# Performance work log

Hardware: AMD Instinct MI355X
Metric: run time of the kernel (lower is better)

## Reference

```python
import jax, jax.numpy as jnp
import numpy as np

N = 50000          # number of nodes / output rows (len(degs))
IN_C, OUT_C = 16, 16
EDGE_F = 13        # edge feature dim fed to filter net
HID = 32           # filter-net hidden width
E_NOMINAL = 800000 # target number of edges (sum of degs)


def setup_inputs() -> dict:
    rng = np.random.default_rng(0)
    # variable per-node degrees in [0, 32], adjusted so they sum exactly to E_NOMINAL
    degs = rng.integers(0, 33, size=N).astype(np.int64)
    degs[0] = max(0, degs[0] + (E_NOMINAL - int(degs.sum())))
    E = int(degs.sum())
    # segment id of each edge = destination node (equivalent to the degs-driven loop)
    idxd = np.repeat(np.arange(N, dtype=np.int32), degs)
    idxn = rng.integers(0, N, size=E).astype(np.int32)  # source node gather index

    key = jax.random.key(0)
    k1, k2, k3, k4 = jax.random.split(key, 4)
    x = jax.random.normal(k1, (N, IN_C), jnp.float32)
    edgefeats = jax.random.normal(k2, (E, EDGE_F), jnp.float32)
    # filter net: Linear(EDGE_F->HID) -> ReLU -> Linear(HID->IN_C*OUT_C)
    W1 = jax.random.normal(k3, (EDGE_F, HID), jnp.float32) / np.float32(np.sqrt(EDGE_F))
    b1 = jnp.zeros((HID,), jnp.float32)
    W2 = jax.random.normal(k4, (HID, IN_C * OUT_C), jnp.float32) / np.float32(np.sqrt(HID))
    b2 = jnp.zeros((IN_C * OUT_C,), jnp.float32)
    return {
        "x": x, "edgefeats": edgefeats,
        "W1": W1, "b1": b1, "W2": W2, "b2": b2,
        "idxn": jnp.asarray(idxn), "idxd": jnp.asarray(idxd),
        "degs": jnp.asarray(degs.astype(np.float32)),
    }


def reference(x, edgefeats, W1, b1, W2, b2, idxn, idxd, degs):
    # filter net generates a per-edge [IN_C, OUT_C] weight matrix
    h = jax.nn.relu(edgefeats @ W1 + b1)                 # [E, HID]
    w = (h @ W2 + b2).reshape(-1, IN_C, OUT_C)           # [E, IN_C, OUT_C]
    # gather source-node features and apply per-edge matvec (bmm with [E,1,IN_C])
    sel = x[idxn]                                        # [E, IN_C]
    prod = jnp.einsum('ei,eio->eo', sel, w)              # [E, OUT_C]
    # segment-mean over each node's incoming edges; degree-0 nodes -> 0
    s = jax.ops.segment_sum(prod, idxd, num_segments=N)  # [N, OUT_C]
    d = degs[:, None]
    return jnp.where(d > 0, s / jnp.maximum(d, 1.0), jnp.float32(0.0))
```

## Files before the change

### kernel.cpp

```cpp
#include <hip/hip_runtime.h>

typedef _Float16 half2v __attribute__((ext_vector_type(2)));
typedef _Float16 half4v __attribute__((ext_vector_type(4)));
typedef _Float16 half8v __attribute__((ext_vector_type(8)));
typedef float   float4v __attribute__((ext_vector_type(4)));

#define INC     16
#define OUTC    16
#define EFN     13
#define HIDC    32
#define EPB     128
#define MAXSPAN 80

#define GLOBAL_AS __attribute__((address_space(1)))
#define LDS_AS    __attribute__((address_space(3)))

union H8 { half8v v; half2v h2[4]; };

__global__ __launch_bounds__(256) void prep(
    const float* __restrict__ W2,
    const float* __restrict__ x,
    _Float16*    __restrict__ wsB,
    _Float16*    __restrict__ wsXh,
    int nh)
{
    const int b = blockIdx.x;
    if (b < 32) {
        const int i = b * 256 + threadIdx.x;
        const int j = i & 7;
        const int l = (i >> 3) & 63;
        const int t = i >> 9;
        const int q = l >> 4, n = l & 15;
        const int kk = (j < 4) ? (q * 4 + j) : (16 + q * 4 + (j & 3));
        wsB[i] = (_Float16)W2[kk * 256 + t * 16 + n];
    } else {
        const int i = (b - 32) * 256 + threadIdx.x;
        if (i * 8 < nh) {
            const float4 v0 = ((const float4*)x)[i * 2];
            const float4 v1 = ((const float4*)x)[i * 2 + 1];
            half8v h;
            h[0] = (_Float16)v0.x; h[1] = (_Float16)v0.y;
            h[2] = (_Float16)v0.z; h[3] = (_Float16)v0.w;
            h[4] = (_Float16)v1.x; h[5] = (_Float16)v1.y;
            h[6] = (_Float16)v1.z; h[7] = (_Float16)v1.w;
            *(half8v*)(wsXh + (size_t)i * 8) = h;
        }
    }
}

__global__ __launch_bounds__(64, 3) void edge_kernel(
    const _Float16* __restrict__ xh,
    const float* __restrict__ edgefeats,
    const float* __restrict__ W1,
    const float* __restrict__ b1,
    const float* __restrict__ b2,
    const int*   __restrict__ idxn,
    const int*   __restrict__ idxd,
    const float* __restrict__ degs,
    const _Float16* __restrict__ wsB,
    float*       __restrict__ out,
    float*       __restrict__ wsPfirst,
    float*       __restrict__ wsPlast,
    int*         __restrict__ wsMeta,
    int E)
{
    __shared__ __align__(16) float sEF[EPB * EFN];
    __shared__ __align__(16) int   sidxn[EPB];
    __shared__ __align__(16) int   sidxd[EPB];
    __shared__ float lacc[MAXSPAN * OUTC];

    const int lane = threadIdx.x;
    const int n    = lane & 15;
    const int q    = lane >> 4;

    const long b0   = (long)blockIdx.x * EPB;
    const long bEnd = (b0 + EPB < (long)E) ? (b0 + EPB) : (long)E;
    const bool full = (b0 + EPB <= (long)E);

    if (full) {
        const char* efsrc = (const char*)edgefeats + (size_t)b0 * (EFN * 4);
        #pragma unroll
        for (int c = 0; c < 6; ++c)
            __builtin_amdgcn_global_load_lds(
                (const GLOBAL_AS unsigned int*)(efsrc + c * 1024 + lane * 16),
                (LDS_AS unsigned int*)((char*)sEF + c * 1024), 16, 0, 0);
        if (lane < 32) {
            __builtin_amdgcn_global_load_lds(
                (const GLOBAL_AS unsigned int*)(efsrc + 6144 + lane * 16),
                (LDS_AS unsigned int*)((char*)sEF + 6144), 16, 0, 0);
            __builtin_amdgcn_global_load_lds(
                (const GLOBAL_AS unsigned int*)((const char*)(idxn + b0) + lane * 16),
                (LDS_AS unsigned int*)sidxn, 16, 0, 0);
            __builtin_amdgcn_global_load_lds(
                (const GLOBAL_AS unsigned int*)((const char*)(idxd + b0) + lane * 16),
                (LDS_AS unsigned int*)sidxd, 16, 0, 0);
        }
    } else {
        const long mx = (long)E * EFN - 1;
        for (int i = lane; i < EPB * EFN; i += 64) {
            long gi = b0 * EFN + i;
            if (gi > mx) gi = mx;
            sEF[i] = edgefeats[gi];
        }
        const long Ec = (long)E - 1;
        for (int i = lane; i < EPB; i += 64) {
            long e = b0 + i;
            if (e > Ec) e = Ec;
            sidxn[i] = idxn[e];
            sidxd[i] = idxd[e];
        }
    }

    const int d_lo = idxd[b0];
    const int d_hi = idxd[bEnd - 1];
    const int span = d_hi - d_lo;

    H8 bfr[16];
    #pragma unroll
    for (int t = 0; t < 16; ++t)
        bfr[t].v = *(const half8v*)(wsB + ((size_t)(t * 64 + lane) * 8));

    #pragma unroll
    for (int it = 0; it < MAXSPAN * OUTC / 64; ++it) lacc[lane + it * 64] = 0.0f;

    half4v a1, a2;
    float4v c1, c2;
    #pragma unroll
    for (int jj = 0; jj < 4; ++jj) {
        const int f = q * 4 + jj;
        const bool ok = (f < EFN);
        a1[jj] = ok ? (_Float16)W1[f * HIDC + n]      : (_Float16)0.f;
        a2[jj] = ok ? (_Float16)W1[f * HIDC + 16 + n] : (_Float16)0.f;
        c1[jj] = b1[q * 4 + jj];
        c2[jj] = b1[16 + q * 4 + jj];
    }
    half8v bfragB2;
    #pragma unroll
    for (int j = 0; j < 8; ++j) {
        _Float16 val = (_Float16)0.f;
        if (q < 2) val = (_Float16)b2[(q * 8 + j) * 16 + n];
        bfragB2[j] = val;
    }

    const int f0i = (q < 3) ? (q * 4) : 9;

    __syncthreads();

    const int nd0 = sidxn[n];
    const int nd1 = sidxn[16 + n];
    half8v pxa0 = *(const half8v*)(xh + (size_t)nd0 * INC);
    half8v pxb0 = *(const half8v*)(xh + (size_t)nd0 * INC + 8);
    half8v pxa1 = *(const half8v*)(xh + (size_t)nd1 * INC);
    half8v pxb1 = *(const half8v*)(xh + (size_t)nd1 * INC + 8);
    __builtin_amdgcn_sched_barrier(0);

    #pragma unroll
    for (int t16 = 0; t16 < 8; ++t16) {
        const long base = b0 + (long)t16 * 16;
        const bool vM   = (base + n < (long)E);

        const half8v xA = (t16 & 1) ? pxa1 : pxa0;
        const half8v xB = (t16 & 1) ? pxb1 : pxb0;
        if (t16 < 6) {
            const int ndn = sidxn[(t16 + 2) * 16 + n];
            if (t16 & 1) {
                pxa1 = *(const half8v*)(xh + (size_t)ndn * INC);
                pxb1 = *(const half8v*)(xh + (size_t)ndn * INC + 8);
            } else {
                pxa0 = *(const half8v*)(xh + (size_t)ndn * INC);
                pxb0 = *(const half8v*)(xh + (size_t)ndn * INC + 8);
            }
        }
        __builtin_amdgcn_sched_barrier(0);

        const int4 dd = *(const int4*)&sidxd[t16 * 16 + q * 4];

        const float* efp = sEF + (size_t)(t16 * 16 + n) * EFN + f0i;
        const float e0 = efp[0], e1 = efp[1], e2 = efp[2], e3 = efp[3];

        H8 sa, sb_;
        sa.v = xA; sb_.v = xB;
        const half2v zz = {(_Float16)0.f, (_Float16)0.f};
        half2v selh[8];
        #pragma unroll
        for (int i = 0; i < 4; ++i) {
            selh[i]     = vM ? sa.h2[i]  : zz;
            selh[4 + i] = vM ? sb_.h2[i] : zz;
        }

        half4v efB;
        if (q < 3) {
            efB[0] = (_Float16)e0; efB[1] = (_Float16)e1;
            efB[2] = (_Float16)e2; efB[3] = (_Float16)e3;
        } else {
            efB[0] = (_Float16)e3; efB[1] = (_Float16)0.f;
            efB[2] = (_Float16)0.f; efB[3] = (_Float16)0.f;
        }

        const float4v hf1 = __builtin_amdgcn_mfma_f32_16x16x16f16(a1, efB, c1, 0, 0, 0);
        const float4v hf2 = __builtin_amdgcn_mfma_f32_16x16x16f16(a2, efB, c2, 0, 0, 0);

        H8 hu;
        #pragma unroll
        for (int r = 0; r < 2; ++r) {
            half2v t1 = {(_Float16)fmaxf(hf1[2*r], 0.f), (_Float16)fmaxf(hf1[2*r+1], 0.f)};
            half2v t2 = {(_Float16)fmaxf(hf2[2*r], 0.f), (_Float16)fmaxf(hf2[2*r+1], 0.f)};
            hu.h2[r]     = t1;
            hu.h2[2 + r] = t2;
        }

        float4v acc = {0.f, 0.f, 0.f, 0.f};
        #pragma unroll
        for (int t = 0; t < 16; ++t) {
            _Float16 sv = (t & 1) ? selh[t >> 1][1] : selh[t >> 1][0];
            half2v sb = {sv, sv};
            H8 a;
            a.h2[0] = sb * hu.h2[0];
            a.h2[1] = sb * hu.h2[1];
            a.h2[2] = sb * hu.h2[2];
            a.h2[3] = sb * hu.h2[3];
            acc = __builtin_amdgcn_mfma_f32_16x16x32_f16(a.v, bfr[t].v, acc, 0, 0, 0);
        }
        {
            H8 a;
            #pragma unroll
            for (int j2 = 0; j2 < 4; ++j2) {
                a.h2[j2] = (q < 2) ? selh[q * 4 + j2] : zz;
            }
            acc = __builtin_amdgcn_mfma_f32_16x16x32_f16(a.v, bfragB2, acc, 0, 0, 0);
        }

        if (dd.x == dd.w) {
            atomicAdd(&lacc[(dd.x - d_lo) * OUTC + n],
                      acc[0] + acc[1] + acc[2] + acc[3]);
        } else {
            atomicAdd(&lacc[(dd.x - d_lo) * OUTC + n], acc[0]);
            atomicAdd(&lacc[(dd.y - d_lo) * OUTC + n], acc[1]);
            atomicAdd(&lacc[(dd.z - d_lo) * OUTC + n], acc[2]);
            atomicAdd(&lacc[(dd.w - d_lo) * OUTC + n], acc[3]);
        }
    }

    __syncthreads();

    const bool first_starts = (b0 == 0)        || (idxd[b0 - 1] != d_lo);
    const bool last_ends    = (bEnd == (long)E) || (idxd[bEnd]   != d_hi);

    for (int i = lane; i < (span + 1) * OUTC; i += 64) {
        const int u = i >> 4;
        const int o = i & 15;
        const int v = d_lo + u;
        const float bin = lacc[u * OUTC + o];
        const bool starts = (u > 0)    || first_starts;
        const bool ends   = (u < span) || last_ends;
        if (starts && ends) {
            const float dg = degs[v];
            out[(size_t)v * OUTC + o] = (dg > 0.0f) ? bin / dg : 0.0f;
        } else if (!starts) {
            wsPfirst[(size_t)blockIdx.x * OUTC + o] = bin;
        } else {
            wsPlast[(size_t)blockIdx.x * OUTC + o] = bin;
        }
    }
    if (lane == 0) {
        wsMeta[blockIdx.x * 4 + 0] = d_hi;
        wsMeta[blockIdx.x * 4 + 1] = last_ends ? 1 : 0;
        wsMeta[blockIdx.x * 4 + 2] =
            (((span > 0) || first_starts) && !last_ends) ? 1 : 0;
    }
}

__global__ __launch_bounds__(256) void fixup_kernel(
    const float* __restrict__ degs,
    float*       __restrict__ out,
    const float* __restrict__ wsPfirst,
    const float* __restrict__ wsPlast,
    const int*   __restrict__ wsMeta,
    int N, int nblocks)
{
    const int t = blockIdx.x * 256 + threadIdx.x;

    if (t < nblocks && wsMeta[t * 4 + 2]) {
        const int v = wsMeta[t * 4 + 0];
        float tot[OUTC];
        #pragma unroll
        for (int o = 0; o < OUTC; ++o) tot[o] = wsPlast[(size_t)t * OUTC + o];
        for (int j = t + 1; j < nblocks; ++j) {
            #pragma unroll
            for (int o = 0; o < OUTC; ++o) tot[o] += wsPfirst[(size_t)j * OUTC + o];
            if (wsMeta[j * 4 + 0] != v || wsMeta[j * 4 + 1]) break;
        }
        const float dg = degs[v];
        #pragma unroll
        for (int o = 0; o < OUTC; ++o) out[(size_t)v * OUTC + o] = tot[o] / dg;
    }

    if (t < N && degs[t] == 0.0f) {
        float4* op = (float4*)(out + (size_t)t * OUTC);
        const float4 z = make_float4(0, 0, 0, 0);
        op[0] = z; op[1] = z; op[2] = z; op[3] = z;
    }
}

extern "C" void kernel_launch(void* const* d_in, const int* in_sizes, int n_in,
                              void* d_out, int out_size, void* d_ws, size_t ws_size,
                              hipStream_t stream)
{
    const float* x         = (const float*)d_in[0];
    const float* edgefeats = (const float*)d_in[1];
    const float* W1        = (const float*)d_in[2];
    const float* b1        = (const float*)d_in[3];
    const float* W2        = (const float*)d_in[4];
    const float* b2        = (const float*)d_in[5];
    const int*   idxn      = (const int*)d_in[6];
    const int*   idxd      = (const int*)d_in[7];
    const float* degs      = (const float*)d_in[8];

    const int E = in_sizes[6];
    const int N = in_sizes[8];
    const int nblocks = (E + EPB - 1) / EPB;
    const int nh = N * INC;

    _Float16* wsB  = (_Float16*)d_ws;
    _Float16* wsXh = (_Float16*)((char*)d_ws + 16384);
    size_t xh_bytes = ((size_t)nh * 2 + 255) & ~(size_t)255;
    float* wsPfirst = (float*)((char*)d_ws + 16384 + xh_bytes);
    float* wsPlast  = wsPfirst + (size_t)nblocks * OUTC;
    int*   wsMeta   = (int*)(wsPlast + (size_t)nblocks * OUTC);

    const int xhblocks = (nh / 8 + 255) / 256;
    prep<<<32 + xhblocks, 256, 0, stream>>>(W2, x, wsB, wsXh, nh);

    edge_kernel<<<nblocks, 64, 0, stream>>>(wsXh, edgefeats, W1, b1, b2,
                                            idxn, idxd, degs, wsB, (float*)d_out,
                                            wsPfirst, wsPlast, wsMeta, E);

    const int fthreads = (N > nblocks) ? N : nblocks;
    fixup_kernel<<<(fthreads + 255) / 256, 256, 0, stream>>>(
        degs, (float*)d_out, wsPfirst, wsPlast, wsMeta, N, nblocks);
}
```

Measured before the change: 158.7 us.

## Gather fp32 x rows directly into LDS and drop the fp16 x conversion pass

Removes the prep step that converted x to fp16 in workspace, so the prep kernel now only packs W2. The edge kernel loads idxn into registers up front and uses async global-to-LDS loads to gather each edge's fp32 source row into shared memory, converting to fp16 after reading it back from LDS. This saves one pass over x and shrinks the pre-kernel, at the cost of more LDS per block (8 KB more, which may affect occupancy) and a gather of twice as many bytes. Tail blocks now zero-fill out-of-range rows in LDS instead of masking them in registers.

```diff
diff --git a/kernel.cpp b/kernel.cpp
--- a/kernel.cpp
+++ b/kernel.cpp
@@ -17,39 +17,20 @@
 
 union H8 { half8v v; half2v h2[4]; };
 
-__global__ __launch_bounds__(256) void prep(
-    const float* __restrict__ W2,
+__global__ __launch_bounds__(256) void pack_w2(const float* __restrict__ W2,
+                                               _Float16* __restrict__ wsB)
+{
+    const int i = blockIdx.x * 256 + threadIdx.x;
+    const int j = i & 7;
+    const int l = (i >> 3) & 63;
+    const int t = i >> 9;
+    const int q = l >> 4, n = l & 15;
+    const int kk = (j < 4) ? (q * 4 + j) : (16 + q * 4 + (j & 3));
+    wsB[i] = (_Float16)W2[kk * 256 + t * 16 + n];
+}
+
+__global__ __launch_bounds__(64, 3) void edge_kernel(
     const float* __restrict__ x,
-    _Float16*    __restrict__ wsB,
-    _Float16*    __restrict__ wsXh,
-    int nh)
-{
-    const int b = blockIdx.x;
-    if (b < 32) {
-        const int i = b * 256 + threadIdx.x;
-        const int j = i & 7;
-        const int l = (i >> 3) & 63;
-        const int t = i >> 9;
-        const int q = l >> 4, n = l & 15;
-        const int kk = (j < 4) ? (q * 4 + j) : (16 + q * 4 + (j & 3));
-        wsB[i] = (_Float16)W2[kk * 256 + t * 16 + n];
-    } else {
-        const int i = (b - 32) * 256 + threadIdx.x;
-        if (i * 8 < nh) {
-            const float4 v0 = ((const float4*)x)[i * 2];
-            const float4 v1 = ((const float4*)x)[i * 2 + 1];
-            half8v h;
-            h[0] = (_Float16)v0.x; h[1] = (_Float16)v0.y;
-            h[2] = (_Float16)v0.z; h[3] = (_Float16)v0.w;
-            h[4] = (_Float16)v1.x; h[5] = (_Float16)v1.y;
-            h[6] = (_Float16)v1.z; h[7] = (_Float16)v1.w;
-            *(half8v*)(wsXh + (size_t)i * 8) = h;
-        }
-    }
-}
-
-__global__ __launch_bounds__(64, 3) void edge_kernel(
-    const _Float16* __restrict__ xh,
     const float* __restrict__ edgefeats,
     const float* __restrict__ W1,
     const float* __restrict__ b1,
@@ -65,7 +46,7 @@
     int E)
 {
     __shared__ __align__(16) float sEF[EPB * EFN];
-    __shared__ __align__(16) int   sidxn[EPB];
+    __shared__ __align__(16) float sX[EPB * INC];
     __shared__ __align__(16) int   sidxd[EPB];
     __shared__ float lacc[MAXSPAN * OUTC];
 
@@ -78,6 +59,12 @@
     const bool full = (b0 + EPB <= (long)E);
 
     if (full) {
+        int nd[8];
+        #pragma unroll
+        for (int t = 0; t < 8; ++t)
+            nd[t] = idxn[b0 + t * 16 + n];
+        __builtin_amdgcn_sched_barrier(0);
+
         const char* efsrc = (const char*)edgefeats + (size_t)b0 * (EFN * 4);
         #pragma unroll
         for (int c = 0; c < 6; ++c)
@@ -89,25 +76,38 @@
                 (const GLOBAL_AS unsigned int*)(efsrc + 6144 + lane * 16),
                 (LDS_AS unsigned int*)((char*)sEF + 6144), 16, 0, 0);
             __builtin_amdgcn_global_load_lds(
-                (const GLOBAL_AS unsigned int*)((const char*)(idxn + b0) + lane * 16),
-                (LDS_AS unsigned int*)sidxn, 16, 0, 0);
-            __builtin_amdgcn_global_load_lds(
                 (const GLOBAL_AS unsigned int*)((const char*)(idxd + b0) + lane * 16),
                 (LDS_AS unsigned int*)sidxd, 16, 0, 0);
         }
+        __builtin_amdgcn_sched_barrier(0);
+
+        #pragma unroll
+        for (int t = 0; t < 8; ++t) {
+            const float* xsrc = x + (size_t)nd[t] * INC + ((lane >> 4) << 2);
+            __builtin_amdgcn_global_load_lds(
+                (const GLOBAL_AS unsigned int*)xsrc,
+                (LDS_AS unsigned int*)((char*)sX + t * 1024), 16, 0, 0);
+        }
     } else {
+        const long Ec = (long)E - 1;
         const long mx = (long)E * EFN - 1;
         for (int i = lane; i < EPB * EFN; i += 64) {
             long gi = b0 * EFN + i;
             if (gi > mx) gi = mx;
             sEF[i] = edgefeats[gi];
         }
-        const long Ec = (long)E - 1;
         for (int i = lane; i < EPB; i += 64) {
-            long e = b0 + i;
-            if (e > Ec) e = Ec;
-            sidxn[i] = idxn[e];
-            sidxd[i] = idxd[e];
+            const long ge = b0 + i;
+            const bool v = (ge <= Ec);
+            sidxd[i] = idxd[v ? ge : Ec];
+            const int ndi = idxn[v ? ge : Ec];
+            const int tt = i >> 4, rr = i & 15;
+            #pragma unroll
+            for (int c = 0; c < 4; ++c) {
+                float4 val = make_float4(0, 0, 0, 0);
+                if (v) val = ((const float4*)(x + (size_t)ndi * INC))[c];
+                *(float4*)((char*)sX + tt * 1024 + c * 256 + rr * 16) = val;
+            }
         }
     }
 
@@ -146,47 +146,28 @@
 
     __syncthreads();
 
-    const int nd0 = sidxn[n];
-    const int nd1 = sidxn[16 + n];
-    half8v pxa0 = *(const half8v*)(xh + (size_t)nd0 * INC);
-    half8v pxb0 = *(const half8v*)(xh + (size_t)nd0 * INC + 8);
-    half8v pxa1 = *(const half8v*)(xh + (size_t)nd1 * INC);
-    half8v pxb1 = *(const half8v*)(xh + (size_t)nd1 * INC + 8);
-    __builtin_amdgcn_sched_barrier(0);
-
     #pragma unroll
     for (int t16 = 0; t16 < 8; ++t16) {
-        const long base = b0 + (long)t16 * 16;
-        const bool vM   = (base + n < (long)E);
-
-        const half8v xA = (t16 & 1) ? pxa1 : pxa0;
-        const half8v xB = (t16 & 1) ? pxb1 : pxb0;
-        if (t16 < 6) {
-            const int ndn = sidxn[(t16 + 2) * 16 + n];
-            if (t16 & 1) {
-                pxa1 = *(const half8v*)(xh + (size_t)ndn * INC);
-                pxb1 = *(const half8v*)(xh + (size_t)ndn * INC + 8);
-            } else {
-                pxa0 = *(const half8v*)(xh + (size_t)ndn * INC);
-                pxb0 = *(const half8v*)(xh + (size_t)ndn * INC + 8);
-            }
-        }
-        __builtin_amdgcn_sched_barrier(0);
-
         const int4 dd = *(const int4*)&sidxd[t16 * 16 + q * 4];
+
+        const char* xt = (const char*)sX + t16 * 1024;
+        const float4 s0 = *(const float4*)(xt + 0 * 256 + n * 16);
+        const float4 s1 = *(const float4*)(xt + 1 * 256 + n * 16);
+        const float4 s2 = *(const float4*)(xt + 2 * 256 + n * 16);
+        const float4 s3 = *(const float4*)(xt + 3 * 256 + n * 16);
 
         const float* efp = sEF + (size_t)(t16 * 16 + n) * EFN + f0i;
         const float e0 = efp[0], e1 = efp[1], e2 = efp[2], e3 = efp[3];
 
-        H8 sa, sb_;
-        sa.v = xA; sb_.v = xB;
-        const half2v zz = {(_Float16)0.f, (_Float16)0.f};
         half2v selh[8];
-        #pragma unroll
-        for (int i = 0; i < 4; ++i) {
-            selh[i]     = vM ? sa.h2[i]  : zz;
-            selh[4 + i] = vM ? sb_.h2[i] : zz;
-        }
+        { half2v t = {(_Float16)s0.x, (_Float16)s0.y}; selh[0] = t; }
+        { half2v t = {(_Float16)s0.z, (_Float16)s0.w}; selh[1] = t; }
+        { half2v t = {(_Float16)s1.x, (_Float16)s1.y}; selh[2] = t; }
+        { half2v t = {(_Float16)s1.z, (_Float16)s1.w}; selh[3] = t; }
+        { half2v t = {(_Float16)s2.x, (_Float16)s2.y}; selh[4] = t; }
+        { half2v t = {(_Float16)s2.z, (_Float16)s2.w}; selh[5] = t; }
+        { half2v t = {(_Float16)s3.x, (_Float16)s3.y}; selh[6] = t; }
+        { half2v t = {(_Float16)s3.z, (_Float16)s3.w}; selh[7] = t; }
 
         half4v efB;
         if (q < 3) {
@@ -223,6 +204,7 @@
         }
         {
             H8 a;
+            const half2v zz = {(_Float16)0.f, (_Float16)0.f};
             #pragma unroll
             for (int j2 = 0; j2 < 4; ++j2) {
                 a.h2[j2] = (q < 2) ? selh[q * 4 + j2] : zz;
@@ -319,19 +301,15 @@
     const int E = in_sizes[6];
     const int N = in_sizes[8];
     const int nblocks = (E + EPB - 1) / EPB;
-    const int nh = N * INC;
-
-    _Float16* wsB  = (_Float16*)d_ws;
-    _Float16* wsXh = (_Float16*)((char*)d_ws + 16384);
-    size_t xh_bytes = ((size_t)nh * 2 + 255) & ~(size_t)255;
-    float* wsPfirst = (float*)((char*)d_ws + 16384 + xh_bytes);
+
+    _Float16* wsB   = (_Float16*)d_ws;
+    float* wsPfirst = (float*)((char*)d_ws + 16384);
     float* wsPlast  = wsPfirst + (size_t)nblocks * OUTC;
     int*   wsMeta   = (int*)(wsPlast + (size_t)nblocks * OUTC);
 
-    const int xhblocks = (nh / 8 + 255) / 256;
-    prep<<<32 + xhblocks, 256, 0, stream>>>(W2, x, wsB, wsXh, nh);
-
-    edge_kernel<<<nblocks, 64, 0, stream>>>(wsXh, edgefeats, W1, b1, b2,
+    pack_w2<<<32, 256, 0, stream>>>(W2, wsB);
+
+    edge_kernel<<<nblocks, 64, 0, stream>>>(x, edgefeats, W1, b1, b2,
                                             idxn, idxd, degs, wsB, (float*)d_out,
                                             wsPfirst, wsPlast, wsMeta, E);
 
```

Measured after the change: 179.0 us. 12.8% more time.

## Pack four independent edge waves per block and drop block-wide barriers

Applied to the files above, without the earlier changes.

The edge kernel now runs four independent 128-edge virtual waves per 256-thread block, each with its own LDS slices. __syncthreads is replaced by per-wave s_waitcnt. The first gather indices come straight from global memory so x loads can start sooner, and the destination indices are read from global instead of being staged in LDS. MAXSPAN is halved and segment rows are clamped to d_hi to keep LDS usage bounded. The aim is to cut per-block overhead and barrier stalls and raise occupancy. The cost is extra global reads for idxd and a risk from the clamp if a chunk spans more than 40 nodes.

```diff
diff --git a/kernel.cpp b/kernel.cpp
--- a/kernel.cpp
+++ b/kernel.cpp
@@ -9,8 +9,9 @@
 #define OUTC    16
 #define EFN     13
 #define HIDC    32
-#define EPB     128
-#define MAXSPAN 80
+#define EPW     128
+#define WPB     4
+#define MAXSPAN 40
 
 #define GLOBAL_AS __attribute__((address_space(1)))
 #define LDS_AS    __attribute__((address_space(3)))
@@ -48,7 +49,7 @@
     }
 }
 
-__global__ __launch_bounds__(64, 3) void edge_kernel(
+__global__ __launch_bounds__(256, 4) void edge_kernel(
     const _Float16* __restrict__ xh,
     const float* __restrict__ edgefeats,
     const float* __restrict__ W1,
@@ -64,18 +65,31 @@
     int*         __restrict__ wsMeta,
     int E)
 {
-    __shared__ __align__(16) float sEF[EPB * EFN];
-    __shared__ __align__(16) int   sidxn[EPB];
-    __shared__ __align__(16) int   sidxd[EPB];
-    __shared__ float lacc[MAXSPAN * OUTC];
-
-    const int lane = threadIdx.x;
+    __shared__ __align__(16) float sEF[WPB][EPW * EFN];
+    __shared__ __align__(16) int   sidxn[WPB][EPW];
+    __shared__ float lacc[WPB][MAXSPAN * OUTC];
+
+    const int tid  = threadIdx.x;
+    const int lane = tid & 63;
+    const int wid  = tid >> 6;
     const int n    = lane & 15;
     const int q    = lane >> 4;
 
-    const long b0   = (long)blockIdx.x * EPB;
-    const long bEnd = (b0 + EPB < (long)E) ? (b0 + EPB) : (long)E;
-    const bool full = (b0 + EPB <= (long)E);
+    const long vw = (long)blockIdx.x * WPB + wid;
+    const long b0 = vw * EPW;
+    if (b0 >= (long)E) return;
+    const long bEnd = (b0 + EPW < (long)E) ? (b0 + EPW) : (long)E;
+    const bool full = (b0 + EPW <= (long)E);
+    const long Em1  = (long)E - 1;
+
+    float* sEF_w   = sEF[wid];
+    int*   sidxn_w = sidxn[wid];
+    float* lacc_w  = lacc[wid];
+
+    const long ea = b0 + n, eb = b0 + 16 + n;
+    const int nd0 = idxn[(ea <= Em1) ? ea : Em1];
+    const int nd1 = idxn[(eb <= Em1) ? eb : Em1];
+    __builtin_amdgcn_sched_barrier(0);
 
     if (full) {
         const char* efsrc = (const char*)edgefeats + (size_t)b0 * (EFN * 4);
@@ -83,33 +97,29 @@
         for (int c = 0; c < 6; ++c)
             __builtin_amdgcn_global_load_lds(
                 (const GLOBAL_AS unsigned int*)(efsrc + c * 1024 + lane * 16),
-                (LDS_AS unsigned int*)((char*)sEF + c * 1024), 16, 0, 0);
+                (LDS_AS unsigned int*)((char*)sEF_w + c * 1024), 16, 0, 0);
         if (lane < 32) {
             __builtin_amdgcn_global_load_lds(
                 (const GLOBAL_AS unsigned int*)(efsrc + 6144 + lane * 16),
-                (LDS_AS unsigned int*)((char*)sEF + 6144), 16, 0, 0);
+                (LDS_AS unsigned int*)((char*)sEF_w + 6144), 16, 0, 0);
             __builtin_amdgcn_global_load_lds(
                 (const GLOBAL_AS unsigned int*)((const char*)(idxn + b0) + lane * 16),
-                (LDS_AS unsigned int*)sidxn, 16, 0, 0);
-            __builtin_amdgcn_global_load_lds(
-                (const GLOBAL_AS unsigned int*)((const char*)(idxd + b0) + lane * 16),
-                (LDS_AS unsigned int*)sidxd, 16, 0, 0);
+                (LDS_AS unsigned int*)sidxn_w, 16, 0, 0);
         }
     } else {
         const long mx = (long)E * EFN - 1;
-        for (int i = lane; i < EPB * EFN; i += 64) {
+        for (int i = lane; i < EPW * EFN; i += 64) {
             long gi = b0 * EFN + i;
             if (gi > mx) gi = mx;
-            sEF[i] = edgefeats[gi];
-        }
-        const long Ec = (long)E - 1;
-        for (int i = lane; i < EPB; i += 64) {
+            sEF_w[i] = edgefeats[gi];
+        }
+        for (int i = lane; i < EPW; i += 64) {
             long e = b0 + i;
-            if (e > Ec) e = Ec;
-            sidxn[i] = idxn[e];
-            sidxd[i] = idxd[e];
-        }
-    }
+            if (e > Em1) e = Em1;
+            sidxn_w[i] = idxn[e];
+        }
+    }
+    __builtin_amdgcn_sched_barrier(0);
 
     const int d_lo = idxd[b0];
     const int d_hi = idxd[bEnd - 1];
@@ -121,7 +131,7 @@
         bfr[t].v = *(const half8v*)(wsB + ((size_t)(t * 64 + lane) * 8));
 
     #pragma unroll
-    for (int it = 0; it < MAXSPAN * OUTC / 64; ++it) lacc[lane + it * 64] = 0.0f;
+    for (int it = 0; it < MAXSPAN * OUTC / 64; ++it) lacc_w[lane + it * 64] = 0.0f;
 
     half4v a1, a2;
     float4v c1, c2;
@@ -144,16 +154,15 @@
 
     const int f0i = (q < 3) ? (q * 4) : 9;
 
-    __syncthreads();
-
-    const int nd0 = sidxn[n];
-    const int nd1 = sidxn[16 + n];
     half8v pxa0 = *(const half8v*)(xh + (size_t)nd0 * INC);
     half8v pxb0 = *(const half8v*)(xh + (size_t)nd0 * INC + 8);
     half8v pxa1 = *(const half8v*)(xh + (size_t)nd1 * INC);
     half8v pxb1 = *(const half8v*)(xh + (size_t)nd1 * INC + 8);
     __builtin_amdgcn_sched_barrier(0);
 
+    asm volatile("s_waitcnt vmcnt(0) lgkmcnt(0)" ::: "memory");
+    __builtin_amdgcn_sched_barrier(0);
+
     #pragma unroll
     for (int t16 = 0; t16 < 8; ++t16) {
         const long base = b0 + (long)t16 * 16;
@@ -162,7 +171,7 @@
         const half8v xA = (t16 & 1) ? pxa1 : pxa0;
         const half8v xB = (t16 & 1) ? pxb1 : pxb0;
         if (t16 < 6) {
-            const int ndn = sidxn[(t16 + 2) * 16 + n];
+            const int ndn = sidxn_w[(t16 + 2) * 16 + n];
             if (t16 & 1) {
                 pxa1 = *(const half8v*)(xh + (size_t)ndn * INC);
                 pxb1 = *(const half8v*)(xh + (size_t)ndn * INC + 8);
@@ -171,11 +180,12 @@
                 pxb0 = *(const half8v*)(xh + (size_t)ndn * INC + 8);
             }
         }
+        long de = base + q * 4;
+        if (de > (long)E - 4) de = (long)E - 4;
+        const int4 dd = *(const int4*)(idxd + de);
         __builtin_amdgcn_sched_barrier(0);
 
-        const int4 dd = *(const int4*)&sidxd[t16 * 16 + q * 4];
-
-        const float* efp = sEF + (size_t)(t16 * 16 + n) * EFN + f0i;
+        const float* efp = sEF_w + (size_t)(t16 * 16 + n) * EFN + f0i;
         const float e0 = efp[0], e1 = efp[1], e2 = efp[2], e3 = efp[3];
 
         H8 sa, sb_;
@@ -230,18 +240,21 @@
             acc = __builtin_amdgcn_mfma_f32_16x16x32_f16(a.v, bfragB2, acc, 0, 0, 0);
         }
 
-        if (dd.x == dd.w) {
-            atomicAdd(&lacc[(dd.x - d_lo) * OUTC + n],
-                      acc[0] + acc[1] + acc[2] + acc[3]);
+        const int r0 = ((dd.x < d_hi) ? dd.x : d_hi) - d_lo;
+        const int r1 = ((dd.y < d_hi) ? dd.y : d_hi) - d_lo;
+        const int r2 = ((dd.z < d_hi) ? dd.z : d_hi) - d_lo;
+        const int r3 = ((dd.w < d_hi) ? dd.w : d_hi) - d_lo;
+        if (r0 == r3) {
+            atomicAdd(&lacc_w[r0 * OUTC + n], acc[0] + acc[1] + acc[2] + acc[3]);
         } else {
-            atomicAdd(&lacc[(dd.x - d_lo) * OUTC + n], acc[0]);
-            atomicAdd(&lacc[(dd.y - d_lo) * OUTC + n], acc[1]);
-            atomicAdd(&lacc[(dd.z - d_lo) * OUTC + n], acc[2]);
-            atomicAdd(&lacc[(dd.w - d_lo) * OUTC + n], acc[3]);
-        }
-    }
-
-    __syncthreads();
+            atomicAdd(&lacc_w[r0 * OUTC + n], acc[0]);
+            atomicAdd(&lacc_w[r1 * OUTC + n], acc[1]);
+            atomicAdd(&lacc_w[r2 * OUTC + n], acc[2]);
+            atomicAdd(&lacc_w[r3 * OUTC + n], acc[3]);
+        }
+    }
+
+    asm volatile("s_waitcnt lgkmcnt(0)" ::: "memory");
 
     const bool first_starts = (b0 == 0)        || (idxd[b0 - 1] != d_lo);
     const bool last_ends    = (bEnd == (long)E) || (idxd[bEnd]   != d_hi);
@@ -250,22 +263,22 @@
         const int u = i >> 4;
         const int o = i & 15;
         const int v = d_lo + u;
-        const float bin = lacc[u * OUTC + o];
+        const float bin = lacc_w[u * OUTC + o];
         const bool starts = (u > 0)    || first_starts;
         const bool ends   = (u < span) || last_ends;
         if (starts && ends) {
             const float dg = degs[v];
             out[(size_t)v * OUTC + o] = (dg > 0.0f) ? bin / dg : 0.0f;
         } else if (!starts) {
-            wsPfirst[(size_t)blockIdx.x * OUTC + o] = bin;
+            wsPfirst[(size_t)vw * OUTC + o] = bin;
         } else {
-            wsPlast[(size_t)blockIdx.x * OUTC + o] = bin;
+            wsPlast[(size_t)vw * OUTC + o] = bin;
         }
     }
     if (lane == 0) {
-        wsMeta[blockIdx.x * 4 + 0] = d_hi;
-        wsMeta[blockIdx.x * 4 + 1] = last_ends ? 1 : 0;
-        wsMeta[blockIdx.x * 4 + 2] =
+        wsMeta[vw * 4 + 0] = d_hi;
+        wsMeta[vw * 4 + 1] = last_ends ? 1 : 0;
+        wsMeta[vw * 4 + 2] =
             (((span > 0) || first_starts) && !last_ends) ? 1 : 0;
     }
 }
@@ -276,16 +289,16 @@
     const float* __restrict__ wsPfirst,
     const float* __restrict__ wsPlast,
     const int*   __restrict__ wsMeta,
-    int N, int nblocks)
+    int N, int nvw)
 {
     const int t = blockIdx.x * 256 + threadIdx.x;
 
-    if (t < nblocks && wsMeta[t * 4 + 2]) {
+    if (t < nvw && wsMeta[t * 4 + 2]) {
         const int v = wsMeta[t * 4 + 0];
         float tot[OUTC];
         #pragma unroll
         for (int o = 0; o < OUTC; ++o) tot[o] = wsPlast[(size_t)t * OUTC + o];
-        for (int j = t + 1; j < nblocks; ++j) {
+        for (int j = t + 1; j < nvw; ++j) {
             #pragma unroll
             for (int o = 0; o < OUTC; ++o) tot[o] += wsPfirst[(size_t)j * OUTC + o];
             if (wsMeta[j * 4 + 0] != v || wsMeta[j * 4 + 1]) break;
@@ -318,24 +331,25 @@
 
     const int E = in_sizes[6];
     const int N = in_sizes[8];
-    const int nblocks = (E + EPB - 1) / EPB;
+    const int nvw   = (E + EPW - 1) / EPW;
+    const int gridw = (nvw + WPB - 1) / WPB;
     const int nh = N * INC;
 
     _Float16* wsB  = (_Float16*)d_ws;
     _Float16* wsXh = (_Float16*)((char*)d_ws + 16384);
     size_t xh_bytes = ((size_t)nh * 2 + 255) & ~(size_t)255;
     float* wsPfirst = (float*)((char*)d_ws + 16384 + xh_bytes);
-    float* wsPlast  = wsPfirst + (size_t)nblocks * OUTC;
-    int*   wsMeta   = (int*)(wsPlast + (size_t)nblocks * OUTC);
+    float* wsPlast  = wsPfirst + (size_t)nvw * OUTC;
+    int*   wsMeta   = (int*)(wsPlast + (size_t)nvw * OUTC);
 
     const int xhblocks = (nh / 8 + 255) / 256;
     prep<<<32 + xhblocks, 256, 0, stream>>>(W2, x, wsB, wsXh, nh);
 
-    edge_kernel<<<nblocks, 64, 0, stream>>>(wsXh, edgefeats, W1, b1, b2,
-                                            idxn, idxd, degs, wsB, (float*)d_out,
-                                            wsPfirst, wsPlast, wsMeta, E);
-
-    const int fthreads = (N > nblocks) ? N : nblocks;
+    edge_kernel<<<gridw, 256, 0, stream>>>(wsXh, edgefeats, W1, b1, b2,
+                                           idxn, idxd, degs, wsB, (float*)d_out,
+                                           wsPfirst, wsPlast, wsMeta, E);
+
+    const int fthreads = (N > nvw) ? N : nvw;
     fixup_kernel<<<(fthreads + 255) / 256, 256, 0, stream>>>(
-        degs, (float*)d_out, wsPfirst, wsPlast, wsMeta, N, nblocks);
+        degs, (float*)d_out, wsPfirst, wsPlast, wsMeta, N, nvw);
 }
```

Measured after the change: 193.0 us. 1.22x slower.
